# Optimization experiments

Measured on AMD Instinct MI355X. Metric: run time of the kernel, lower is better.

The kernel has to match this reference:

```python
import jax, jax.numpy as jnp
import numpy as np
import math

KSIZE = 7
CHANNELS = 256


def setup_inputs() -> dict:
    key = jax.random.key(0)
    k1, k2, k3, k4 = jax.random.split(key, 4)
    B, C, H, W = 8, CHANNELS, 256, 256
    x = jax.random.normal(k1, (B, C, H, W), dtype=jnp.float32)
    # torch defaults: log_sigma = log(1)=0, log_freq = log(0.2), theta = 0; add small noise
    log_sigma = 0.0 + 0.05 * jax.random.normal(k2, (C,), dtype=jnp.float32)
    log_freq = jnp.float32(math.log(0.2)) + 0.05 * jax.random.normal(k3, (C,), dtype=jnp.float32)
    theta = 0.05 * jax.random.normal(k4, (C,), dtype=jnp.float32)
    return {"x": x, "log_sigma": log_sigma, "log_freq": log_freq, "theta": theta}


def _gabor_kernels(log_sigma, log_freq, theta, dtype):
    """Vectorized per-channel Gabor kernel synthesis. Returns [C, 1, k, k]."""
    half = KSIZE // 2
    r = jnp.arange(-half, half + 1, dtype=dtype)
    gx, gy = jnp.meshgrid(r, r, indexing="ij")  # [k, k]
    sigma = jnp.exp(log_sigma)[:, None, None]   # [C,1,1]
    freq = jnp.exp(log_freq)[:, None, None]
    c = jnp.cos(theta)[:, None, None]
    s = jnp.sin(theta)[:, None, None]
    # xy = grid @ rot.T / sigma, with rot = [[c, s], [-s, c]] so rot.T = [[c, -s], [s, c]]
    x0 = (gx[None] * c + gy[None] * s) / sigma    # [C,k,k]
    x1 = (-gx[None] * s + gy[None] * c) / sigma   # [C,k,k]
    gauss = jnp.exp(-(x0 * x0 + x1 * x1) / 2)
    kern = gauss * jnp.cos(2 * jnp.pi * freq * x0)
    kern = kern / jnp.sum(kern, axis=(1, 2), keepdims=True)
    return kern[:, None]  # [C,1,k,k]


def reference(x, log_sigma, log_freq, theta):
    C = x.shape[1]
    weight = _gabor_kernels(log_sigma, log_freq, theta, x.dtype)
    pad = KSIZE // 2
    # depthwise conv (groups=C); NOTE: original forward omits stride, so stride=1
    out = jax.lax.conv_general_dilated(
        x, weight,
        window_strides=(1, 1),
        padding=[(pad, pad), (pad, pad)],
        dimension_numbers=("NCHW", "OIHW", "NCHW"),
        feature_group_count=C,
    )
    return out
```

## Files before the change

kernel.cpp:

```cpp
#include <hip/hip_runtime.h>
#include <math.h>

#define KSIZE 7
#define C_CH  256
#define HW    256
#define BATCH 8

#define TH    32
#define ROWS  (TH + 6)
#define LDW   264
#define NT    (HW / TH)

__global__ void gabor_weights_kernel(const float* __restrict__ log_sigma,
                                     const float* __restrict__ log_freq,
                                     const float* __restrict__ theta,
                                     float* __restrict__ gw) {
    int c = threadIdx.x;
    if (c >= C_CH) return;
    float sigma = expf(log_sigma[c]);
    float freq  = expf(log_freq[c]);
    float ct = cosf(theta[c]);
    float st = sinf(theta[c]);
    float inv_sigma = 1.0f / sigma;
    float vals[KSIZE * KSIZE];
    float sum = 0.0f;
    #pragma unroll
    for (int i = 0; i < KSIZE; ++i) {
        #pragma unroll
        for (int j = 0; j < KSIZE; ++j) {
            float dx = (float)(i - 3);
            float dy = (float)(j - 3);
            float x0 = (dx * ct + dy * st) * inv_sigma;
            float x1 = (-dx * st + dy * ct) * inv_sigma;
            float g  = expf(-0.5f * (x0 * x0 + x1 * x1));
            float v  = g * cosf(6.283185307179586f * freq * x0);
            vals[i * KSIZE + j] = v;
            sum += v;
        }
    }
    float inv = 1.0f / sum;
    #pragma unroll
    for (int k = 0; k < KSIZE * KSIZE; ++k)
        gw[c * (KSIZE * KSIZE) + k] = vals[k] * inv;
}

__device__ __forceinline__ void gload_lds16(const float* g, float* l) {
    __builtin_amdgcn_global_load_lds(
        (const __attribute__((address_space(1))) void*)g,
        (__attribute__((address_space(3))) void*)l,
        16, 0, 0);
}

__global__ __launch_bounds__(256, 2)
void gabor_conv_kernel(const float* __restrict__ x,
                       const float* __restrict__ gw,
                       float* __restrict__ out) {
    __shared__ float tile[2][ROWS][LDW];

    const int tid  = threadIdx.x;
    const int lane = tid & 63;
    const int wv   = tid >> 6;
    const int c    = blockIdx.x;
    const int n    = blockIdx.y;

    const size_t plane = ((size_t)n * C_CH + c) * (size_t)(HW * HW);
    const float* xp = x + plane;
    float*       op = out + plane;

    for (int idx = tid; idx < 2 * ROWS; idx += 256) {
        int b  = idx / ROWS;
        int rr = idx - b * ROWS;
        *reinterpret_cast<float4*>(&tile[b][rr][0])   = make_float4(0.f, 0.f, 0.f, 0.f);
        *reinterpret_cast<float4*>(&tile[b][rr][260]) = make_float4(0.f, 0.f, 0.f, 0.f);
    }

    float w[KSIZE * KSIZE];
    const float* wp = gw + c * (KSIZE * KSIZE);
    #pragma unroll
    for (int k = 0; k < KSIZE * KSIZE; ++k) w[k] = wp[k];

#define STAGE(BUF, T) do {                                                   \
        const int row0_ = (T) * TH - 3;                                      \
        for (int rr = wv; rr < ROWS; rr += 4) {                              \
            int gr = row0_ + rr;                                             \
            if (gr >= 0 && gr < HW) {                                        \
                gload_lds16(xp + (size_t)gr * HW + lane * 4,                 \
                            &tile[BUF][rr][4]);                              \
            } else {                                                         \
                *reinterpret_cast<float4*>(&tile[BUF][rr][4 + lane * 4]) =   \
                    make_float4(0.f, 0.f, 0.f, 0.f);                         \
            }                                                                \
        }                                                                    \
    } while (0)

    STAGE(0, 0);
    __syncthreads();

    const int colp = lane * 4;
    const int ob   = wv * 8;

    for (int t = 0; t < NT; ++t) {
        const int cur = t & 1;

        if (t + 1 < NT) STAGE(cur ^ 1, t + 1);

        float acc[8][4];
        #pragma unroll
        for (int o = 0; o < 8; ++o)
            #pragma unroll
            for (int cc = 0; cc < 4; ++cc) acc[o][cc] = 0.f;

        #pragma unroll
        for (int r = 0; r < 14; ++r) {
            float4 a = *reinterpret_cast<const float4*>(&tile[cur][ob + r][colp]);
            float4 b = *reinterpret_cast<const float4*>(&tile[cur][ob + r][colp + 4]);
            float4 d = *reinterpret_cast<const float4*>(&tile[cur][ob + r][colp + 8]);
            float f[12] = {a.x, a.y, a.z, a.w, b.x, b.y, b.z, b.w, d.x, d.y, d.z, d.w};
            #pragma unroll
            for (int o = 0; o < 8; ++o) {
                if (o <= r && r <= o + 6) {
                    const int ki = r - o;
                    #pragma unroll
                    for (int cc = 0; cc < 4; ++cc) {
                        #pragma unroll
                        for (int j = 0; j < KSIZE; ++j)
                            acc[o][cc] += f[cc + j + 1] * w[ki * KSIZE + j];
                    }
                }
            }
        }

        const int orow0 = t * TH + ob;
        #pragma unroll
        for (int o = 0; o < 8; ++o) {
            float4 v = make_float4(acc[o][0], acc[o][1], acc[o][2], acc[o][3]);
            *reinterpret_cast<float4*>(op + (size_t)(orow0 + o) * HW + colp) = v;
        }

        __syncthreads();
    }
#undef STAGE
}

extern "C" void kernel_launch(void* const* d_in, const int* in_sizes, int n_in,
                              void* d_out, int out_size, void* d_ws, size_t ws_size,
                              hipStream_t stream) {
    const float* x  = (const float*)d_in[0];
    const float* ls = (const float*)d_in[1];
    const float* lf = (const float*)d_in[2];
    const float* th = (const float*)d_in[3];
    float* out = (float*)d_out;
    float* gw  = (float*)d_ws;

    gabor_weights_kernel<<<1, 256, 0, stream>>>(ls, lf, th, gw);

    dim3 grid(C_CH, BATCH);
    gabor_conv_kernel<<<grid, 256, 0, stream>>>(x, gw, out);
}
```

Measured before the change: 282.0 us.

## Reuse halo rows across row tiles in LDS and relax end-of-tile wait

The six overlapping halo rows at the bottom of the current LDS tile are copied into the top of the next buffer instead of being reloaded from global memory. Only the new rows are fetched, and zero padding is written explicitly at the image top and bottom. The end-of-iteration __syncthreads is replaced by s_waitcnt vmcnt(8) plus a raw barrier, so the eight output stores can stay in flight while the prefetched loads are waited on. This cuts redundant global reads of the input. In exchange it adds LDS copy traffic and depends on vmcnt ordering loads and stores in issue order.

```diff
diff --git a/kernel.cpp b/kernel.cpp
--- a/kernel.cpp
+++ b/kernel.cpp
@@ -79,30 +79,42 @@
     #pragma unroll
     for (int k = 0; k < KSIZE * KSIZE; ++k) w[k] = wp[k];
 
-#define STAGE(BUF, T) do {                                                   \
-        const int row0_ = (T) * TH - 3;                                      \
-        for (int rr = wv; rr < ROWS; rr += 4) {                              \
-            int gr = row0_ + rr;                                             \
-            if (gr >= 0 && gr < HW) {                                        \
-                gload_lds16(xp + (size_t)gr * HW + lane * 4,                 \
-                            &tile[BUF][rr][4]);                              \
-            } else {                                                         \
-                *reinterpret_cast<float4*>(&tile[BUF][rr][4 + lane * 4]) =   \
-                    make_float4(0.f, 0.f, 0.f, 0.f);                         \
-            }                                                                \
-        }                                                                    \
-    } while (0)
-
-    STAGE(0, 0);
-    __syncthreads();
+    for (int i = tid; i < 3 * 64; i += 256) {
+        int r = i >> 6, q = i & 63;
+        *reinterpret_cast<float4*>(&tile[0][r][4 + q * 4]) = make_float4(0.f, 0.f, 0.f, 0.f);
+    }
+    for (int rr = 3 + wv; rr < ROWS; rr += 4)
+        gload_lds16(xp + (size_t)(rr - 3) * HW + lane * 4, &tile[0][rr][4]);
+    asm volatile("s_waitcnt vmcnt(0) lgkmcnt(0)" ::: "memory");
+    __builtin_amdgcn_s_barrier();
 
     const int colp = lane * 4;
     const int ob   = wv * 8;
 
     for (int t = 0; t < NT; ++t) {
         const int cur = t & 1;
+        const int nxt = cur ^ 1;
 
-        if (t + 1 < NT) STAGE(cur ^ 1, t + 1);
+        if (t + 1 < NT) {
+            for (int i = tid; i < 6 * 64; i += 256) {
+                int r = i >> 6, q = i & 63;
+                *reinterpret_cast<float4*>(&tile[nxt][r][4 + q * 4]) =
+                    *reinterpret_cast<const float4*>(&tile[cur][32 + r][4 + q * 4]);
+            }
+            if (t + 1 == NT - 1) {
+                for (int i = tid; i < 3 * 64; i += 256) {
+                    int r = 35 + (i >> 6), q = i & 63;
+                    *reinterpret_cast<float4*>(&tile[nxt][r][4 + q * 4]) =
+                        make_float4(0.f, 0.f, 0.f, 0.f);
+                }
+            }
+            const int row0 = (t + 1) * TH - 3;
+            const int rmax = (t + 1 == NT - 1) ? 34 : 37;
+            for (int rr = 6 + wv; rr <= rmax; rr += 4)
+                gload_lds16(xp + (size_t)(row0 + rr) * HW + lane * 4,
+                            &tile[nxt][rr][4]);
+        }
+        asm volatile("" ::: "memory");
 
         float acc[8][4];
         #pragma unroll
@@ -137,9 +149,11 @@
             *reinterpret_cast<float4*>(op + (size_t)(orow0 + o) * HW + colp) = v;
         }
 
-        __syncthreads();
+        if (t + 1 < NT) {
+            asm volatile("s_waitcnt vmcnt(8) lgkmcnt(0)" ::: "memory");
+            __builtin_amdgcn_s_barrier();
+        }
     }
-#undef STAGE
 }
 
 extern "C" void kernel_launch(void* const* d_in, const int* in_sizes, int n_in,
```

After: 281.1 us. No clear change (-0.3%).
